# Kernel tuning notes

Hardware: AMD Instinct MI355X
Metric: run time of the kernel (lower is better)

## Reference

```python
import jax, jax.numpy as jnp
import numpy as np

OUT, IN, BLK = 11008, 4096, 128

def setup_inputs() -> dict:
    key = jax.random.key(0)
    k1, k2, k3, k4, k5 = jax.random.split(key, 5)
    x = jax.random.normal(k1, (64, IN), dtype=jnp.float32)
    weight = jax.random.randint(k2, (OUT, IN // 2), 0, 256, dtype=jnp.int32)  # packed uint4 pairs
    scale = jax.random.uniform(k3, (OUT, 1, BLK), dtype=jnp.float32) * 0.01 + 1e-4
    zp = jax.random.randint(k4, (OUT, 1, BLK), 0, 16).astype(jnp.float32)
    bias = jax.random.normal(k5, (OUT,), dtype=jnp.float32)
    return {"x": x, "weight": weight, "scale": scale, "zp": zp, "bias": bias}

def reference(x, weight, scale, zp, bias):
    dtype = x.dtype
    # unpack: high nibble first, then low nibble (interleaved along in_features)
    w_h = (weight >> 4) & 15
    w_l = weight & 15
    w_unpacked = jnp.stack((w_h, w_l), axis=-1).reshape(OUT, IN)
    # block-wise dequant: scale/zp shaped [OUT, 1, BLK], broadcast over block index dim
    w_blocked = w_unpacked.reshape(OUT, IN // BLK, BLK).astype(dtype)
    w_rec = ((w_blocked - zp.astype(dtype)) * scale.astype(dtype)).reshape(OUT, IN)
    return x @ w_rec.T + bias
```

## Files before the change

### kernel.cpp

```cpp
#include <hip/hip_runtime.h>

#define OUT_F 11008
#define IN_F  4096
#define PKW   2048
#define BLKQ  128

typedef __attribute__((ext_vector_type(8))) short          s16x8;
typedef __attribute__((ext_vector_type(8))) unsigned short u16x8;
typedef __attribute__((ext_vector_type(4))) float          f32x4;
typedef __attribute__((ext_vector_type(4))) int            i32x4;

__device__ __forceinline__ unsigned short f2bf(float f) {
    union { float f; unsigned u; } v; v.f = f;
    unsigned r = v.u + 0x8000u + ((v.u >> 16) & 1u);
    return (unsigned short)(r >> 16);
}

__global__ void prep_xfrag(const float* __restrict__ x, unsigned short* __restrict__ xf) {
    int kb   = blockIdx.x;
    int t    = threadIdx.x;
    int mt   = t >> 6;
    int lane = t & 63;
    int m  = mt * 16 + (lane & 15);
    int k0 = kb * 32 + (lane >> 4) * 8;
    const float* xp = x + m * IN_F + k0;
    f32x4 a = *(const f32x4*)(xp);
    f32x4 b = *(const f32x4*)(xp + 4);
    u16x8 v;
    v[0] = f2bf(a[0]); v[1] = f2bf(a[1]); v[2] = f2bf(a[2]); v[3] = f2bf(a[3]);
    v[4] = f2bf(b[0]); v[5] = f2bf(b[1]); v[6] = f2bf(b[2]); v[7] = f2bf(b[3]);
    *(u16x8*)(xf + (size_t)((kb * 4 + mt) * 64 + lane) * 8) = v;
}

__global__ __launch_bounds__(512, 4) void qlin_main(
    const int*   __restrict__ wq,
    const float* __restrict__ scale,
    const float* __restrict__ zp,
    const float* __restrict__ bias,
    const unsigned short* __restrict__ xf,
    float* __restrict__ out)
{
    __shared__ float lsum[8 * 1024];

    const int t      = threadIdx.x;
    const int o_base = blockIdx.x * 16;
    const int wave   = t >> 6;
    const int lane   = t & 63;
    const int o_r    = lane & 15;
    const int quad   = lane >> 4;
    const int o      = o_base + o_r;
    const int kh     = wave >> 2;
    const int ph     = wave & 3;

    float s[8], zs[8];
    {
        const float* sp  = scale + (size_t)o * BLKQ + ph * 32 + quad * 8;
        const float* zpp = zp    + (size_t)o * BLKQ + ph * 32 + quad * 8;
        f32x4 s0 = *(const f32x4*)(sp);
        f32x4 s1 = *(const f32x4*)(sp + 4);
        f32x4 z0 = *(const f32x4*)(zpp);
        f32x4 z1 = *(const f32x4*)(zpp + 4);
        #pragma unroll
        for (int i = 0; i < 4; ++i) {
            s [i]     = s0[i];  zs[i]     = z0[i] * s0[i];
            s [i + 4] = s1[i];  zs[i + 4] = z1[i] * s1[i];
        }
    }

    const int* wqp = wq + (size_t)o * PKW + (kh * 64 + ph) * 16 + quad * 4;
    const s16x8* xfp = (const s16x8*)xf + (size_t)(kh * 64 + ph) * 256 + lane;

    f32x4 acc0 = {0.f,0.f,0.f,0.f}, acc1 = acc0, acc2 = acc0, acc3 = acc0;
    s16x8 afA0, afA1, afA2, afA3, afB0, afB1, afB2, afB3;
    i32x4 wg0, wg1, wg2, wg3;

    afA0 = xfp[0];    afA1 = xfp[64];        afA2 = xfp[128];        afA3 = xfp[192];
    afB0 = xfp[1024]; afB1 = xfp[1024 + 64]; afB2 = xfp[1024 + 128]; afB3 = xfp[1024 + 192];
    wg0 = *(const i32x4*)(wqp);
    wg1 = *(const i32x4*)(wqp + 64);
    wg2 = *(const i32x4*)(wqp + 128);
    wg3 = *(const i32x4*)(wqp + 192);

#define SUB(J, A0, A1, A2, A3) do {                                              \
        s16x8 bfr;                                                               \
        _Pragma("unroll")                                                        \
        for (int d = 0; d < 4; ++d) {                                            \
            unsigned dw = (unsigned)wg##J[d];                                    \
            float fh = (float)((dw >> 4) & 15u);       \
            float fl = (float)(dw & 15u);                             \
            bfr[2 * d]     = (short)f2bf(fmaf(fh, s[2 * d],     -zs[2 * d]));    \
            bfr[2 * d + 1] = (short)f2bf(fmaf(fl, s[2 * d + 1], -zs[2 * d + 1]));\
        }                                                                        \
        acc0 = __builtin_amdgcn_mfma_f32_16x16x32_bf16(A0, bfr, acc0, 0, 0, 0);  \
        acc1 = __builtin_amdgcn_mfma_f32_16x16x32_bf16(A1, bfr, acc1, 0, 0, 0);  \
        acc2 = __builtin_amdgcn_mfma_f32_16x16x32_bf16(A2, bfr, acc2, 0, 0, 0);  \
        acc3 = __builtin_amdgcn_mfma_f32_16x16x32_bf16(A3, bfr, acc3, 0, 0, 0);  \
        if (tp + (J) + 2 < 16) {                                                 \
            const s16x8* ap_ = xfp + (size_t)(tp + (J) + 2) * 1024;              \
            A0 = ap_[0]; A1 = ap_[64]; A2 = ap_[128]; A3 = ap_[192];             \
        }                                                                        \
        if (tp + (J) + 4 < 16) {                                                 \
            wg##J = *(const i32x4*)(wqp + (tp + (J) + 4) * 64);                  \
        }                                                                        \
    } while (0)

    for (int tp = 0; tp < 16; tp += 4) {
        SUB(0, afA0, afA1, afA2, afA3);
        SUB(1, afB0, afB1, afB2, afB3);
        SUB(2, afA0, afA1, afA2, afA3);
        SUB(3, afB0, afB1, afB2, afB3);
    }
#undef SUB

    {
        const int mb = quad * 4;
#define STACC(MT, A)                                                  \
        lsum[wave * 1024 + ((MT) * 16 + mb + 0) * 16 + o_r] = A[0];   \
        lsum[wave * 1024 + ((MT) * 16 + mb + 1) * 16 + o_r] = A[1];   \
        lsum[wave * 1024 + ((MT) * 16 + mb + 2) * 16 + o_r] = A[2];   \
        lsum[wave * 1024 + ((MT) * 16 + mb + 3) * 16 + o_r] = A[3];
        STACC(0, acc0) STACC(1, acc1) STACC(2, acc2) STACC(3, acc3)
#undef STACC
    }
    __syncthreads();
    #pragma unroll
    for (int p = 0; p < 2; ++p) {
        int e = p * 512 + t;
        int m = e >> 4, col = e & 15;
        float v = lsum[e]        + lsum[1024 + e] + lsum[2048 + e] + lsum[3072 + e]
                + lsum[4096 + e] + lsum[5120 + e] + lsum[6144 + e] + lsum[7168 + e]
                + bias[o_base + col];
        out[(size_t)m * OUT_F + o_base + col] = v;
    }
}

extern "C" void kernel_launch(void* const* d_in, const int* in_sizes, int n_in,
                              void* d_out, int out_size, void* d_ws, size_t ws_size,
                              hipStream_t stream) {
    const float* x     = (const float*)d_in[0];
    const int*   wq    = (const int*)d_in[1];
    const float* scale = (const float*)d_in[2];
    const float* zpv   = (const float*)d_in[3];
    const float* bias  = (const float*)d_in[4];
    float* out = (float*)d_out;
    unsigned short* xf = (unsigned short*)d_ws;

    prep_xfrag<<<128, 256, 0, stream>>>(x, xf);
    qlin_main<<<OUT_F / 16, 512, 0, stream>>>(wq, scale, zpv, bias, xf, out);
}
```

Before: 169.1 us.

## Stream weights through per-wave LDS ring via global_load_lds with explicit vmcnt pipeline

Weight loads now go asynchronously into a per-wave 4-slot LDS ring using global_load_lds, and activation fragments are held in a 4-deep register ring. Each round issues loads three rounds ahead and waits with explicit s_waitcnt vmcnt counts, and sched_barriers fix the instruction order. The K split across waves is also changed: each wave now handles a contiguous 16-dword slice per 128-dword stride instead of the previous kh/ph split. The aim is deeper memory-latency hiding for this bandwidth-bound int4 GEMV. In exchange it relies on hand-tuned waitcnt values and adds an LDS round trip for the weights.

Result: slower. 202.7 us (+19.8%).

```diff
diff --git a/kernel.cpp b/kernel.cpp
--- a/kernel.cpp
+++ b/kernel.cpp
@@ -9,6 +9,9 @@
 typedef __attribute__((ext_vector_type(8))) unsigned short u16x8;
 typedef __attribute__((ext_vector_type(4))) float          f32x4;
 typedef __attribute__((ext_vector_type(4))) int            i32x4;
+
+#define STR_(x) #x
+#define XSTR(x) STR_(x)
 
 __device__ __forceinline__ unsigned short f2bf(float f) {
     union { float f; unsigned u; } v; v.f = f;
@@ -32,6 +35,11 @@
     *(u16x8*)(xf + (size_t)((kb * 4 + mt) * 64 + lane) * 8) = v;
 }
 
+union SmT {
+    unsigned char ring[8][4][1024];
+    float         lsum[8192];
+};
+
 __global__ __launch_bounds__(512, 4) void qlin_main(
     const int*   __restrict__ wq,
     const float* __restrict__ scale,
@@ -40,7 +48,7 @@
     const unsigned short* __restrict__ xf,
     float* __restrict__ out)
 {
-    __shared__ float lsum[8 * 1024];
+    __shared__ SmT sm;
 
     const int t      = threadIdx.x;
     const int o_base = blockIdx.x * 16;
@@ -49,13 +57,11 @@
     const int o_r    = lane & 15;
     const int quad   = lane >> 4;
     const int o      = o_base + o_r;
-    const int kh     = wave >> 2;
-    const int ph     = wave & 3;
 
     float s[8], zs[8];
     {
-        const float* sp  = scale + (size_t)o * BLKQ + ph * 32 + quad * 8;
-        const float* zpp = zp    + (size_t)o * BLKQ + ph * 32 + quad * 8;
+        const float* sp  = scale + (size_t)o * BLKQ + (wave & 3) * 32 + quad * 8;
+        const float* zpp = zp    + (size_t)o * BLKQ + (wave & 3) * 32 + quad * 8;
         f32x4 s0 = *(const f32x4*)(sp);
         f32x4 s1 = *(const f32x4*)(sp + 4);
         f32x4 z0 = *(const f32x4*)(zpp);
@@ -67,58 +73,66 @@
         }
     }
 
-    const int* wqp = wq + (size_t)o * PKW + (kh * 64 + ph) * 16 + quad * 4;
-    const s16x8* xfp = (const s16x8*)xf + (size_t)(kh * 64 + ph) * 256 + lane;
+    const int* wgS = wq + (size_t)o * PKW + wave * 16 + quad * 4;
+    const char* xfB = (const char*)xf + (size_t)wave * 4096 + (size_t)lane * 16;
+    unsigned char* ringw = &sm.ring[wave][0][0];
 
     f32x4 acc0 = {0.f,0.f,0.f,0.f}, acc1 = acc0, acc2 = acc0, acc3 = acc0;
-    s16x8 afA0, afA1, afA2, afA3, afB0, afB1, afB2, afB3;
-    i32x4 wg0, wg1, wg2, wg3;
+    s16x8 afb[4][4];
 
-    afA0 = xfp[0];    afA1 = xfp[64];        afA2 = xfp[128];        afA3 = xfp[192];
-    afB0 = xfp[1024]; afB1 = xfp[1024 + 64]; afB2 = xfp[1024 + 128]; afB3 = xfp[1024 + 192];
-    wg0 = *(const i32x4*)(wqp);
-    wg1 = *(const i32x4*)(wqp + 64);
-    wg2 = *(const i32x4*)(wqp + 128);
-    wg3 = *(const i32x4*)(wqp + 192);
-
-#define SUB(J, A0, A1, A2, A3) do {                                              \
-        s16x8 bfr;                                                               \
-        _Pragma("unroll")                                                        \
-        for (int d = 0; d < 4; ++d) {                                            \
-            unsigned dw = (unsigned)wg##J[d];                                    \
-            float fh = (float)((dw >> 4) & 15u);       \
-            float fl = (float)(dw & 15u);                             \
-            bfr[2 * d]     = (short)f2bf(fmaf(fh, s[2 * d],     -zs[2 * d]));    \
-            bfr[2 * d + 1] = (short)f2bf(fmaf(fl, s[2 * d + 1], -zs[2 * d + 1]));\
-        }                                                                        \
-        acc0 = __builtin_amdgcn_mfma_f32_16x16x32_bf16(A0, bfr, acc0, 0, 0, 0);  \
-        acc1 = __builtin_amdgcn_mfma_f32_16x16x32_bf16(A1, bfr, acc1, 0, 0, 0);  \
-        acc2 = __builtin_amdgcn_mfma_f32_16x16x32_bf16(A2, bfr, acc2, 0, 0, 0);  \
-        acc3 = __builtin_amdgcn_mfma_f32_16x16x32_bf16(A3, bfr, acc3, 0, 0, 0);  \
-        if (tp + (J) + 2 < 16) {                                                 \
-            const s16x8* ap_ = xfp + (size_t)(tp + (J) + 2) * 1024;              \
-            A0 = ap_[0]; A1 = ap_[64]; A2 = ap_[128]; A3 = ap_[192];             \
-        }                                                                        \
-        if (tp + (J) + 4 < 16) {                                                 \
-            wg##J = *(const i32x4*)(wqp + (tp + (J) + 4) * 64);                  \
-        }                                                                        \
+#define ISSUE(R) do {                                                           \
+        __builtin_amdgcn_global_load_lds(                                       \
+            (const __attribute__((address_space(1))) int*)(wgS + (R) * 128),    \
+            (__attribute__((address_space(3))) int*)(ringw + ((R) & 3) * 1024), \
+            16, 0, 0);                                                          \
+        const s16x8* ap_ = (const s16x8*)(xfB + (size_t)(R) * 32768);           \
+        afb[(R) & 3][0] = ap_[0];                                               \
+        afb[(R) & 3][1] = ap_[64];                                              \
+        afb[(R) & 3][2] = ap_[128];                                             \
+        afb[(R) & 3][3] = ap_[192];                                             \
     } while (0)
 
-    for (int tp = 0; tp < 16; tp += 4) {
-        SUB(0, afA0, afA1, afA2, afA3);
-        SUB(1, afB0, afB1, afB2, afB3);
-        SUB(2, afA0, afA1, afA2, afA3);
-        SUB(3, afB0, afB1, afB2, afB3);
-    }
-#undef SUB
+#define RND(R, WN, DOISS) do {                                                  \
+        if (DOISS) ISSUE((R) + 3);                                              \
+        __builtin_amdgcn_sched_barrier(0);                                      \
+        asm volatile("s_waitcnt vmcnt(" XSTR(WN) ")");                          \
+        __builtin_amdgcn_sched_barrier(0);                                      \
+        i32x4 wreg = *(const i32x4*)(ringw + ((R) & 3) * 1024 + lane * 16);     \
+        s16x8 bfr;                                                              \
+        _Pragma("unroll")                                                       \
+        for (int d = 0; d < 4; ++d) {                                           \
+            unsigned dw = (unsigned)wreg[d];                                    \
+            float fh = (float)((dw >> 4) & 15u);      \
+            float fl = (float)(dw & 15u);                            \
+            bfr[2 * d]     = (short)f2bf(fmaf(fh, s[2 * d],     -zs[2 * d]));   \
+            bfr[2 * d + 1] = (short)f2bf(fmaf(fl, s[2 * d + 1], -zs[2 * d + 1]));\
+        }                                                                       \
+        acc0 = __builtin_amdgcn_mfma_f32_16x16x32_bf16(afb[(R) & 3][0], bfr, acc0, 0, 0, 0); \
+        acc1 = __builtin_amdgcn_mfma_f32_16x16x32_bf16(afb[(R) & 3][1], bfr, acc1, 0, 0, 0); \
+        acc2 = __builtin_amdgcn_mfma_f32_16x16x32_bf16(afb[(R) & 3][2], bfr, acc2, 0, 0, 0); \
+        acc3 = __builtin_amdgcn_mfma_f32_16x16x32_bf16(afb[(R) & 3][3], bfr, acc3, 0, 0, 0); \
+        __builtin_amdgcn_sched_barrier(0);                                      \
+    } while (0)
+
+    ISSUE(0); __builtin_amdgcn_sched_barrier(0);
+    ISSUE(1); __builtin_amdgcn_sched_barrier(0);
+    ISSUE(2); __builtin_amdgcn_sched_barrier(0);
+
+    RND( 0, 15, 1);  RND( 1, 15, 1);  RND( 2, 15, 1);  RND( 3, 15, 1);
+    RND( 4, 15, 1);  RND( 5, 15, 1);  RND( 6, 15, 1);  RND( 7, 15, 1);
+    RND( 8, 15, 1);  RND( 9, 15, 1);  RND(10, 15, 1);  RND(11, 15, 1);
+    RND(12, 15, 1);  RND(13, 10, 0);  RND(14,  5, 0);  RND(15,  0, 0);
+
+#undef RND
+#undef ISSUE
 
     {
         const int mb = quad * 4;
-#define STACC(MT, A)                                                  \
-        lsum[wave * 1024 + ((MT) * 16 + mb + 0) * 16 + o_r] = A[0];   \
-        lsum[wave * 1024 + ((MT) * 16 + mb + 1) * 16 + o_r] = A[1];   \
-        lsum[wave * 1024 + ((MT) * 16 + mb + 2) * 16 + o_r] = A[2];   \
-        lsum[wave * 1024 + ((MT) * 16 + mb + 3) * 16 + o_r] = A[3];
+#define STACC(MT, A)                                                      \
+        sm.lsum[wave * 1024 + ((MT) * 16 + mb + 0) * 16 + o_r] = A[0];    \
+        sm.lsum[wave * 1024 + ((MT) * 16 + mb + 1) * 16 + o_r] = A[1];    \
+        sm.lsum[wave * 1024 + ((MT) * 16 + mb + 2) * 16 + o_r] = A[2];    \
+        sm.lsum[wave * 1024 + ((MT) * 16 + mb + 3) * 16 + o_r] = A[3];
         STACC(0, acc0) STACC(1, acc1) STACC(2, acc2) STACC(3, acc3)
 #undef STACC
     }
@@ -127,8 +141,8 @@
     for (int p = 0; p < 2; ++p) {
         int e = p * 512 + t;
         int m = e >> 4, col = e & 15;
-        float v = lsum[e]        + lsum[1024 + e] + lsum[2048 + e] + lsum[3072 + e]
-                + lsum[4096 + e] + lsum[5120 + e] + lsum[6144 + e] + lsum[7168 + e]
+        float v = sm.lsum[e]        + sm.lsum[1024 + e] + sm.lsum[2048 + e] + sm.lsum[3072 + e]
+                + sm.lsum[4096 + e] + sm.lsum[5120 + e] + sm.lsum[6144 + e] + sm.lsum[7168 + e]
                 + bias[o_base + col];
         out[(size_t)m * OUT_F + o_base + col] = v;
     }
```
